# Performance work log

Measured on AMD Instinct MI355X. Metric: run time of the kernel, lower is better.

The kernel has to match this reference:

```python
import jax, jax.numpy as jnp
import numpy as np

K = 8  # knn_k
EPS = 1e-5


def _grid_edges(H, W):
    # 4-connectivity grid edges, both directions. Returns (src, tgt) numpy int arrays.
    idx = np.arange(H * W).reshape(H, W)
    right_a, right_b = idx[:, :-1].ravel(), idx[:, 1:].ravel()
    down_a, down_b = idx[:-1, :].ravel(), idx[1:, :].ravel()
    src = np.concatenate([right_a, right_b, down_a, down_b])
    tgt = np.concatenate([right_b, right_a, down_b, down_a])
    return src.astype(np.int32), tgt.astype(np.int32)


def setup_inputs() -> dict:
    key = jax.random.key(0)
    k1, _ = jax.random.split(key)
    feature_map = jax.random.normal(k1, (16, 256, 48, 48), dtype=jnp.float32)
    gamma = jnp.ones((256,), jnp.float32)
    beta = jnp.zeros((256,), jnp.float32)
    return {"feature_map": feature_map, "gamma": gamma, "beta": beta}


def reference(feature_map, gamma, beta):
    B, C, H, W = feature_map.shape
    N = H * W
    # flatten_feature_map: [B,C,H,W] -> [B,N,C]
    nodes = feature_map.reshape(B, C, N).transpose(0, 2, 1)

    # static grid edges (4-connectivity)
    g_src_np, g_tgt_np = _grid_edges(H, W)
    g_src = jnp.asarray(g_src_np)
    g_tgt = jnp.asarray(g_tgt_np)

    # feature-space kNN per sample (cdist + topk); exclude self with large diag
    big_diag = jnp.eye(N, dtype=nodes.dtype) * 1e9

    def knn_idx(x):  # x: [N, C]
        sq = jnp.sum(x * x, axis=1)
        d2 = sq[:, None] + sq[None, :] - 2.0 * (x @ x.T) + big_diag
        _, idx = jax.lax.top_k(-d2, K)  # [N, K] nearest neighbors
        return idx

    knn_src = jax.vmap(knn_idx)(nodes).reshape(B, N * K)  # per-sample sources
    knn_tgt = jnp.repeat(jnp.arange(N, dtype=jnp.int32), K)  # static targets

    tgt_all = jnp.concatenate([g_tgt, knn_tgt])  # same for all samples
    n_edges = tgt_all.shape[0]
    ones = jnp.ones((n_edges,), nodes.dtype)

    def aggregate(x, k_src):  # mean over incoming edges (fallback path)
        src_all = jnp.concatenate([g_src, k_src.astype(jnp.int32)])
        agg = jax.ops.segment_sum(x[src_all], tgt_all, num_segments=N)
        cnt = jax.ops.segment_sum(ones, tgt_all, num_segments=N)
        return agg / jnp.clip(cnt, 1.0)[:, None]

    refined = jax.vmap(aggregate)(nodes, knn_src)  # [B, N, C]

    # residual + LayerNorm over channel dim
    y = refined + nodes
    mu = jnp.mean(y, axis=-1, keepdims=True)
    var = jnp.mean((y - mu) ** 2, axis=-1, keepdims=True)
    y = (y - mu) * jax.lax.rsqrt(var + EPS) * gamma + beta

    # unflatten: [B,N,C] -> [B,C,H,W]
    return y.transpose(0, 2, 1).reshape(B, C, H, W)
```

## Files before the change

kernel.cpp:

```cpp
#include <hip/hip_runtime.h>

#define B_   16
#define C_   256
#define H_   48
#define W_   48
#define N_   (H_ * W_)
#define KNN  8

#define NG   (N_ / 32)
#define NT   17
#define FRAG 512
#define MPRE 10
#define NCAND 20

typedef __attribute__((ext_vector_type(8)))  short bf16x8;
typedef __attribute__((ext_vector_type(8)))  unsigned short u16x8;
typedef __attribute__((ext_vector_type(16))) float f32x16;

__device__ __forceinline__ unsigned short f2bf(float f) {
    unsigned int u = __float_as_uint(f);
    u = (u + 0x7FFF + ((u >> 16) & 1)) >> 16;
    return (unsigned short)u;
}
__device__ __forceinline__ float bf2f(unsigned short h) {
    return __uint_as_float(((unsigned int)h) << 16);
}
__device__ __forceinline__ bool lex_lt(float v, int i, float bv, int bi) {
    return (v < bv) || (v == bv && i < bi);
}
__device__ __forceinline__ unsigned int f2sort(float f) {
    unsigned int u = __float_as_uint(f);
    return u ^ ((unsigned int)((int)u >> 31) | 0x80000000u);
}

__global__ __launch_bounds__(256) void k_transpose(const float* __restrict__ fm,
                                                   float* __restrict__ nodes,
                                                   unsigned short* __restrict__ Xf) {
    __shared__ float tile[32][33];
    int b  = blockIdx.z;
    int n0 = blockIdx.x * 32;
    int c0 = blockIdx.y * 32;
    int tx = threadIdx.x, ty = threadIdx.y;
    const float* src = fm + (size_t)b * C_ * N_;
    float* dst = nodes + (size_t)b * N_ * C_;
    #pragma unroll
    for (int cc = 0; cc < 32; cc += 8)
        tile[cc + ty][tx] = src[(size_t)(c0 + cc + ty) * N_ + n0 + tx];
    __syncthreads();
    #pragma unroll
    for (int nn = 0; nn < 32; nn += 8)
        dst[(size_t)(n0 + nn + ty) * C_ + c0 + tx] = tile[tx][nn + ty];

    int flat = ty * 32 + tx;
    int wv = flat >> 6, lane = flat & 63;
    if (wv < 2) {
        int t   = 2 * blockIdx.y + wv;
        int l31 = lane & 31, lh = lane >> 5;
        u16x8 o;
        #pragma unroll
        for (int e = 0; e < 8; ++e)
            o[e] = f2bf(tile[wv * 16 + lh * 8 + e][l31]);
        unsigned short* df = Xf + (((size_t)b * NG + blockIdx.x) * NT + t) * FRAG + lane * 8;
        *(u16x8*)df = o;
    }
}

__global__ __launch_bounds__(256) void k_sq(const float* __restrict__ fm,
                                            float* __restrict__ sq,
                                            unsigned short* __restrict__ Xf) {
    int b = blockIdx.y;
    int n = blockIdx.x * 256 + threadIdx.x;
    const float* src = fm + (size_t)b * C_ * N_ + n;
    float s = 0.f;
    for (int c = 0; c < C_; ++c) { float v = src[(size_t)c * N_]; s = fmaf(v, v, s); }
    sq[b * N_ + n] = s;

    float sh = -0.5f * s;
    unsigned short e1 = f2bf(sh);
    unsigned short e2 = f2bf(sh - bf2f(e1));
    int g = n >> 5, l = n & 31;
    unsigned short* df = Xf + (((size_t)b * NG + g) * NT + 16) * FRAG + l * 8;
    u16x8 o = (u16x8){0, 0, 0, 0, 0, 0, 0, 0};
    o[0] = e1; o[1] = e2;
    *(u16x8*)df = o;
    u16x8 z = (u16x8){0, 0, 0, 0, 0, 0, 0, 0};
    *(u16x8*)(df + 32 * 8) = z;
}

__global__ __launch_bounds__(512) void k_knn_mfma(const unsigned short* __restrict__ Xf,
                                                  int* __restrict__ pi_pre) {
    __shared__ unsigned int ms[2][4][32][MPRE];

    int bid  = blockIdx.x;
    int wgid = (bid & 7) * 72 + (bid >> 3);
    int b    = wgid / 36;
    int i0   = (wgid % 36) * 64;

    int tid = threadIdx.x;
    int wave = tid >> 6, lane = tid & 63;
    int wi = wave & 1, wj = wave >> 1;
    int l31 = lane & 31, lh = lane >> 5;

    const unsigned short* Xb = Xf + (size_t)b * NG * NT * FRAG;
    int gi = (i0 >> 5) + wi;

    bf16x8 bfr[16];
    const unsigned short* ibase = Xb + (size_t)gi * NT * FRAG + lane * 8;
    #pragma unroll
    for (int t = 0; t < 16; ++t) bfr[t] = *(const bf16x8*)(ibase + t * FRAG);
    short one = (lh == 0) ? (short)0x3F80 : (short)0;
    bf16x8 bc = (bf16x8){one, one, 0, 0, 0, 0, 0, 0};

    int I0 = i0 + wi * 32 + l31;

    unsigned int best[MPRE];
    #pragma unroll
    for (int q = 0; q < MPRE; ++q) best[q] = 0u;

    for (int jt = 0; jt < 18; ++jt) {
        int gj = jt * 4 + wj;
        const unsigned short* ab = Xb + (size_t)gj * NT * FRAG + lane * 8;

        f32x16 acc;
        #pragma unroll
        for (int r = 0; r < 16; ++r) acc[r] = 0.f;

        #pragma unroll
        for (int t = 0; t < 16; ++t) {
            bf16x8 af = *(const bf16x8*)(ab + t * FRAG);
            acc = __builtin_amdgcn_mfma_f32_32x32x16_bf16(af, bfr[t], acc, 0, 0, 0);
        }
        {
            bf16x8 af = *(const bf16x8*)(ab + 16 * FRAG);
            acc = __builtin_amdgcn_mfma_f32_32x32x16_bf16(af, bc, acc, 0, 0, 0);
        }

        int j0 = gj * 32;
        int idxbase = 4095 - j0 - 4 * lh;
        #pragma unroll
        for (int r = 0; r < 16; ++r) {
            int cr = (r & 3) + 8 * (r >> 2);
            int gjrow = j0 + cr + 4 * lh;
            unsigned int p = (f2sort(acc[r]) & 0xFFFFF000u) | (unsigned int)(idxbase - cr);
            p = (gjrow == I0) ? 0u : p;
            #pragma unroll
            for (int q = 0; q < MPRE; ++q) {
                unsigned int hi = p > best[q] ? p : best[q];
                unsigned int lo = p > best[q] ? best[q] : p;
                best[q] = hi; p = lo;
            }
        }
    }

    {
        unsigned int part[MPRE];
        #pragma unroll
        for (int q = 0; q < MPRE; ++q)
            part[q] = (unsigned int)__shfl_xor((int)best[q], 32);
        #pragma unroll
        for (int q = 0; q < MPRE; ++q) {
            unsigned int p = part[q];
            #pragma unroll
            for (int s = 0; s < MPRE; ++s) {
                unsigned int hi = p > best[s] ? p : best[s];
                unsigned int lo = p > best[s] ? best[s] : p;
                best[s] = hi; p = lo;
            }
        }
    }
    if (lh == 0) {
        #pragma unroll
        for (int q = 0; q < MPRE; ++q) ms[wi][wj][l31][q] = best[q];
    }
    __syncthreads();

    if (tid < 64) {
        int mwi = tid >> 5, mcol = tid & 31;
        unsigned int mb[NCAND];
        #pragma unroll
        for (int q = 0; q < NCAND; ++q) mb[q] = 0u;
        for (int wjj = 0; wjj < 4; ++wjj) {
            #pragma unroll
            for (int qq = 0; qq < MPRE; ++qq) {
                unsigned int p = ms[mwi][wjj][mcol][qq];
                #pragma unroll
                for (int q = 0; q < NCAND; ++q) {
                    unsigned int hi = p > mb[q] ? p : mb[q];
                    unsigned int lo = p > mb[q] ? mb[q] : p;
                    mb[q] = hi; p = lo;
                }
            }
        }
        int i_g = i0 + tid;
        int* dst = pi_pre + ((size_t)b * N_ + i_g) * NCAND;
        #pragma unroll
        for (int q = 0; q < NCAND; ++q) dst[q] = 4095 - (int)(mb[q] & 0xFFFu);
    }
}

__global__ __launch_bounds__(256) void k_rerank(const float* __restrict__ nodes,
                                                const float* __restrict__ sq,
                                                const int* __restrict__ pi_pre,
                                                int* __restrict__ knn) {
    __shared__ float d2s[4][NCAND];
    __shared__ int   jss[4][NCAND];

    int wv   = threadIdx.x >> 6;
    int lane = threadIdx.x & 63;
    int row  = blockIdx.x * 4 + wv;
    int g = lane >> 4, m = lane & 15;
    int b = row / N_;
    const float* Xb = nodes + (size_t)b * N_ * C_;
    const float* xi = nodes + (size_t)row * C_;

    float4 xiv[4];
    #pragma unroll
    for (int p = 0; p < 4; ++p) xiv[p] = *(const float4*)&xi[p * 64 + m * 4];
    float sqi = sq[row];
    const int* cand = pi_pre + (size_t)row * NCAND;

    for (int it = 0; it < 5; ++it) {
        int c = it * 4 + g;
        int j = cand[c];
        bool valid = (unsigned)j < (unsigned)N_;
        int jc = valid ? j : 0;
        const float* xj = Xb + (size_t)jc * C_;
        float p = 0.f;
        #pragma unroll
        for (int pp = 0; pp < 4; ++pp) {
            float4 v = *(const float4*)&xj[pp * 64 + m * 4];
            p = fmaf(xiv[pp].x, v.x, p);
            p = fmaf(xiv[pp].y, v.y, p);
            p = fmaf(xiv[pp].z, v.z, p);
            p = fmaf(xiv[pp].w, v.w, p);
        }
        p += __shfl_xor(p, 1);
        p += __shfl_xor(p, 2);
        p += __shfl_xor(p, 4);
        p += __shfl_xor(p, 8);
        if (m == 0) {
            float d2 = valid ? (sqi + sq[b * N_ + jc] - 2.f * p) : 3.4e38f;
            d2s[wv][c] = d2;
            jss[wv][c] = valid ? j : 0x7fffffff;
        }
    }

    float bd[KNN]; int bj[KNN];
    #pragma unroll
    for (int q = 0; q < KNN; ++q) { bd[q] = 3.4e38f; bj[q] = 0x7fffffff; }
    for (int s = 0; s < NCAND; ++s) {
        float v = d2s[wv][s]; int jx = jss[wv][s];
        if (lex_lt(v, jx, bd[KNN - 1], bj[KNN - 1])) {
            float cv = v; int ci = jx;
            #pragma unroll
            for (int q = 0; q < KNN; ++q) {
                if (lex_lt(cv, ci, bd[q], bj[q])) {
                    float tv = bd[q]; bd[q] = cv; cv = tv;
                    int tx2 = bj[q]; bj[q] = ci; ci = tx2;
                }
            }
        }
    }
    if (lane == 0) {
        int* kr = knn + (size_t)row * KNN;
        #pragma unroll
        for (int q = 0; q < KNN; ++q) kr[q] = bj[q];
    }
}

__global__ __launch_bounds__(256) void k_agg_ln(const float* __restrict__ nodes,
                                                const int* __restrict__ knn,
                                                const float* __restrict__ gamma,
                                                const float* __restrict__ beta,
                                                float* __restrict__ out) {
    __shared__ float ytile[16][C_ + 1];

    int b   = blockIdx.y;
    int i0  = blockIdx.x * 16;
    int tid = threadIdx.x;
    int wv = tid >> 6, lane = tid & 63;
    const float* Xb = nodes + (size_t)b * N_ * C_;

    float4 g4 = *(const float4*)&gamma[lane * 4];
    float4 b4 = *(const float4*)&beta[lane * 4];

    for (int rr = 0; rr < 4; ++rr) {
        int ii = wv * 4 + rr;
        int i  = i0 + ii;
        int x_ = i % W_;
        int y_ = i / W_;
        float s0 = 0.f, s1 = 0.f, s2 = 0.f, s3 = 0.f;
        int cnt = KNN;

        #define ADDROW(J) { float4 v = *(const float4*)&Xb[(size_t)(J) * C_ + lane * 4]; \
                            s0 += v.x; s1 += v.y; s2 += v.z; s3 += v.w; }
        if (x_ > 0)      { ADDROW(i - 1);  cnt++; }
        if (x_ < W_ - 1) { ADDROW(i + 1);  cnt++; }
        if (y_ > 0)      { ADDROW(i - W_); cnt++; }
        if (y_ < H_ - 1) { ADDROW(i + W_); cnt++; }
        const int* kr = knn + ((size_t)b * N_ + i) * KNN;
        #pragma unroll
        for (int k = 0; k < KNN; ++k) ADDROW(kr[k]);
        #undef ADDROW

        float4 xi = *(const float4*)&Xb[(size_t)i * C_ + lane * 4];
        float ic = 1.f / (float)cnt;
        float y0 = s0 * ic + xi.x;
        float y1 = s1 * ic + xi.y;
        float y2 = s2 * ic + xi.z;
        float y3 = s3 * ic + xi.w;

        float rx = y0 + y1 + y2 + y3;
        float ry = y0 * y0 + y1 * y1 + y2 * y2 + y3 * y3;
        #pragma unroll
        for (int mm = 1; mm < 64; mm <<= 1) {
            rx += __shfl_xor(rx, mm);
            ry += __shfl_xor(ry, mm);
        }
        float mu  = rx * (1.f / C_);
        float var = ry * (1.f / C_) - mu * mu;
        float inv = rsqrtf(var + 1e-5f);

        ytile[ii][lane * 4 + 0] = (y0 - mu) * inv * g4.x + b4.x;
        ytile[ii][lane * 4 + 1] = (y1 - mu) * inv * g4.y + b4.y;
        ytile[ii][lane * 4 + 2] = (y2 - mu) * inv * g4.z + b4.z;
        ytile[ii][lane * 4 + 3] = (y3 - mu) * inv * g4.w + b4.w;
    }
    __syncthreads();

    float* op = out + (size_t)b * C_ * N_ + (size_t)tid * N_ + i0;
    float vv[16];
    #pragma unroll
    for (int ii = 0; ii < 16; ++ii) vv[ii] = ytile[ii][tid];
    #pragma unroll
    for (int q = 0; q < 4; ++q) {
        float4 w;
        w.x = vv[q * 4 + 0]; w.y = vv[q * 4 + 1];
        w.z = vv[q * 4 + 2]; w.w = vv[q * 4 + 3];
        *(float4*)&op[q * 4] = w;
    }
}

extern "C" void kernel_launch(void* const* d_in, const int* in_sizes, int n_in,
                              void* d_out, int out_size, void* d_ws, size_t ws_size,
                              hipStream_t stream) {
    const float* fm    = (const float*)d_in[0];
    const float* gamma = (const float*)d_in[1];
    const float* beta  = (const float*)d_in[2];
    float* out = (float*)d_out;

    char* ws = (char*)d_ws;
    size_t off = 0;
    float* nodes = (float*)(ws + off); off += (size_t)B_ * N_ * C_ * sizeof(float);
    float* sq    = (float*)(ws + off); off += (size_t)B_ * N_ * sizeof(float);
    int*   knn   = (int*)  (ws + off); off += (size_t)B_ * N_ * KNN * sizeof(int);
    unsigned short* Xf = (unsigned short*)(ws + off);
    off += (size_t)B_ * NG * NT * FRAG * sizeof(unsigned short);
    int* pi_pre = (int*)(ws + off);
    off += (size_t)B_ * N_ * NCAND * sizeof(int);

    k_transpose<<<dim3(N_ / 32, C_ / 32, B_), dim3(32, 8), 0, stream>>>(fm, nodes, Xf);
    k_sq<<<dim3(N_ / 256, B_), 256, 0, stream>>>(fm, sq, Xf);
    k_knn_mfma<<<(B_ * N_) / 64, 512, 0, stream>>>(Xf, pi_pre);
    k_rerank<<<(B_ * N_) / 4, 256, 0, stream>>>(nodes, sq, pi_pre, knn);
    k_agg_ln<<<dim3(N_ / 16, B_), 256, 0, stream>>>(nodes, knn, gamma, beta, out);
}
```

Measured before the change: 345.9 us.

## Fuse rerank into aggregation, shrink kNN blocks, drop sort-key conversion via bias

Merges the candidate rerank kernel into the aggregation/LayerNorm kernel so the selected neighbor indices stay in registers instead of round-tripping through global memory, removing one launch. The kNN MFMA kernel now uses 256-thread blocks covering a single 32-row group. A constant bias is injected through the extra MFMA column so scores can be compared as raw float bits, skipping the sign-fixing sort-key transform. This relies on all biased scores being non-negative; if not, ordering of candidates may be wrong.

```diff
diff --git a/kernel.cpp b/kernel.cpp
--- a/kernel.cpp
+++ b/kernel.cpp
@@ -27,10 +27,6 @@
 }
 __device__ __forceinline__ bool lex_lt(float v, int i, float bv, int bi) {
     return (v < bv) || (v == bv && i < bi);
-}
-__device__ __forceinline__ unsigned int f2sort(float f) {
-    unsigned int u = __float_as_uint(f);
-    return u ^ ((unsigned int)((int)u >> 31) | 0x80000000u);
 }
 
 __global__ __launch_bounds__(256) void k_transpose(const float* __restrict__ fm,
@@ -81,37 +77,35 @@
     int g = n >> 5, l = n & 31;
     unsigned short* df = Xf + (((size_t)b * NG + g) * NT + 16) * FRAG + l * 8;
     u16x8 o = (u16x8){0, 0, 0, 0, 0, 0, 0, 0};
-    o[0] = e1; o[1] = e2;
+    o[0] = e1; o[1] = e2; o[2] = 0x4400;
     *(u16x8*)df = o;
     u16x8 z = (u16x8){0, 0, 0, 0, 0, 0, 0, 0};
     *(u16x8*)(df + 32 * 8) = z;
 }
 
-__global__ __launch_bounds__(512) void k_knn_mfma(const unsigned short* __restrict__ Xf,
+__global__ __launch_bounds__(256) void k_knn_mfma(const unsigned short* __restrict__ Xf,
                                                   int* __restrict__ pi_pre) {
-    __shared__ unsigned int ms[2][4][32][MPRE];
+    __shared__ unsigned int ms[4][32][MPRE];
 
     int bid  = blockIdx.x;
-    int wgid = (bid & 7) * 72 + (bid >> 3);
-    int b    = wgid / 36;
-    int i0   = (wgid % 36) * 64;
+    int wgid = (bid & 7) * 144 + (bid >> 3);
+    int b    = wgid / NG;
+    int ig   = wgid % NG;
 
     int tid = threadIdx.x;
-    int wave = tid >> 6, lane = tid & 63;
-    int wi = wave & 1, wj = wave >> 1;
+    int wj = tid >> 6, lane = tid & 63;
     int l31 = lane & 31, lh = lane >> 5;
 
     const unsigned short* Xb = Xf + (size_t)b * NG * NT * FRAG;
-    int gi = (i0 >> 5) + wi;
 
     bf16x8 bfr[16];
-    const unsigned short* ibase = Xb + (size_t)gi * NT * FRAG + lane * 8;
+    const unsigned short* ibase = Xb + (size_t)ig * NT * FRAG + lane * 8;
     #pragma unroll
     for (int t = 0; t < 16; ++t) bfr[t] = *(const bf16x8*)(ibase + t * FRAG);
     short one = (lh == 0) ? (short)0x3F80 : (short)0;
-    bf16x8 bc = (bf16x8){one, one, 0, 0, 0, 0, 0, 0};
-
-    int I0 = i0 + wi * 32 + l31;
+    bf16x8 bc = (bf16x8){one, one, one, 0, 0, 0, 0, 0};
+
+    int I0 = ig * 32 + l31;
 
     unsigned int best[MPRE];
     #pragma unroll
@@ -141,7 +135,8 @@
         for (int r = 0; r < 16; ++r) {
             int cr = (r & 3) + 8 * (r >> 2);
             int gjrow = j0 + cr + 4 * lh;
-            unsigned int p = (f2sort(acc[r]) & 0xFFFFF000u) | (unsigned int)(idxbase - cr);
+            unsigned int p = (__float_as_uint(acc[r]) & 0xFFFFF000u)
+                           | (unsigned int)(idxbase - cr);
             p = (gjrow == I0) ? 0u : p;
             #pragma unroll
             for (int q = 0; q < MPRE; ++q) {
@@ -170,19 +165,18 @@
     }
     if (lh == 0) {
         #pragma unroll
-        for (int q = 0; q < MPRE; ++q) ms[wi][wj][l31][q] = best[q];
+        for (int q = 0; q < MPRE; ++q) ms[wj][l31][q] = best[q];
     }
     __syncthreads();
 
-    if (tid < 64) {
-        int mwi = tid >> 5, mcol = tid & 31;
+    if (tid < 32) {
         unsigned int mb[NCAND];
         #pragma unroll
         for (int q = 0; q < NCAND; ++q) mb[q] = 0u;
         for (int wjj = 0; wjj < 4; ++wjj) {
             #pragma unroll
             for (int qq = 0; qq < MPRE; ++qq) {
-                unsigned int p = ms[mwi][wjj][mcol][qq];
+                unsigned int p = ms[wjj][tid][qq];
                 #pragma unroll
                 for (int q = 0; q < NCAND; ++q) {
                     unsigned int hi = p > mb[q] ? p : mb[q];
@@ -191,124 +185,107 @@
                 }
             }
         }
-        int i_g = i0 + tid;
+        int i_g = ig * 32 + tid;
         int* dst = pi_pre + ((size_t)b * N_ + i_g) * NCAND;
         #pragma unroll
         for (int q = 0; q < NCAND; ++q) dst[q] = 4095 - (int)(mb[q] & 0xFFFu);
     }
 }
 
-__global__ __launch_bounds__(256) void k_rerank(const float* __restrict__ nodes,
-                                                const float* __restrict__ sq,
-                                                const int* __restrict__ pi_pre,
-                                                int* __restrict__ knn) {
+__global__ __launch_bounds__(256) void k_rerank_agg(const float* __restrict__ nodes,
+                                                    const float* __restrict__ sq,
+                                                    const int* __restrict__ pi_pre,
+                                                    const float* __restrict__ gamma,
+                                                    const float* __restrict__ beta,
+                                                    float* __restrict__ out) {
     __shared__ float d2s[4][NCAND];
     __shared__ int   jss[4][NCAND];
-
-    int wv   = threadIdx.x >> 6;
-    int lane = threadIdx.x & 63;
-    int row  = blockIdx.x * 4 + wv;
-    int g = lane >> 4, m = lane & 15;
-    int b = row / N_;
-    const float* Xb = nodes + (size_t)b * N_ * C_;
-    const float* xi = nodes + (size_t)row * C_;
-
-    float4 xiv[4];
-    #pragma unroll
-    for (int p = 0; p < 4; ++p) xiv[p] = *(const float4*)&xi[p * 64 + m * 4];
-    float sqi = sq[row];
-    const int* cand = pi_pre + (size_t)row * NCAND;
-
-    for (int it = 0; it < 5; ++it) {
-        int c = it * 4 + g;
-        int j = cand[c];
-        bool valid = (unsigned)j < (unsigned)N_;
-        int jc = valid ? j : 0;
-        const float* xj = Xb + (size_t)jc * C_;
-        float p = 0.f;
-        #pragma unroll
-        for (int pp = 0; pp < 4; ++pp) {
-            float4 v = *(const float4*)&xj[pp * 64 + m * 4];
-            p = fmaf(xiv[pp].x, v.x, p);
-            p = fmaf(xiv[pp].y, v.y, p);
-            p = fmaf(xiv[pp].z, v.z, p);
-            p = fmaf(xiv[pp].w, v.w, p);
-        }
-        p += __shfl_xor(p, 1);
-        p += __shfl_xor(p, 2);
-        p += __shfl_xor(p, 4);
-        p += __shfl_xor(p, 8);
-        if (m == 0) {
-            float d2 = valid ? (sqi + sq[b * N_ + jc] - 2.f * p) : 3.4e38f;
-            d2s[wv][c] = d2;
-            jss[wv][c] = valid ? j : 0x7fffffff;
-        }
-    }
-
-    float bd[KNN]; int bj[KNN];
-    #pragma unroll
-    for (int q = 0; q < KNN; ++q) { bd[q] = 3.4e38f; bj[q] = 0x7fffffff; }
-    for (int s = 0; s < NCAND; ++s) {
-        float v = d2s[wv][s]; int jx = jss[wv][s];
-        if (lex_lt(v, jx, bd[KNN - 1], bj[KNN - 1])) {
-            float cv = v; int ci = jx;
-            #pragma unroll
-            for (int q = 0; q < KNN; ++q) {
-                if (lex_lt(cv, ci, bd[q], bj[q])) {
-                    float tv = bd[q]; bd[q] = cv; cv = tv;
-                    int tx2 = bj[q]; bj[q] = ci; ci = tx2;
-                }
-            }
-        }
-    }
-    if (lane == 0) {
-        int* kr = knn + (size_t)row * KNN;
-        #pragma unroll
-        for (int q = 0; q < KNN; ++q) kr[q] = bj[q];
-    }
-}
-
-__global__ __launch_bounds__(256) void k_agg_ln(const float* __restrict__ nodes,
-                                                const int* __restrict__ knn,
-                                                const float* __restrict__ gamma,
-                                                const float* __restrict__ beta,
-                                                float* __restrict__ out) {
     __shared__ float ytile[16][C_ + 1];
 
-    int b   = blockIdx.y;
-    int i0  = blockIdx.x * 16;
-    int tid = threadIdx.x;
-    int wv = tid >> 6, lane = tid & 63;
+    int tid  = threadIdx.x;
+    int wv   = tid >> 6, lane = tid & 63;
+    int g    = lane >> 4, m = lane & 15;
+    int row0 = blockIdx.x * 16;
+    int b    = row0 / N_;
+    int i0   = row0 - b * N_;
     const float* Xb = nodes + (size_t)b * N_ * C_;
 
     float4 g4 = *(const float4*)&gamma[lane * 4];
     float4 b4 = *(const float4*)&beta[lane * 4];
 
     for (int rr = 0; rr < 4; ++rr) {
-        int ii = wv * 4 + rr;
-        int i  = i0 + ii;
+        int i    = i0 + wv * 4 + rr;
+        int rowg = b * N_ + i;
+
+        const float* xi = Xb + (size_t)i * C_;
+        float4 xiv[4];
+        #pragma unroll
+        for (int p = 0; p < 4; ++p) xiv[p] = *(const float4*)&xi[p * 64 + m * 4];
+        float sqi = sq[rowg];
+        const int* cand = pi_pre + (size_t)rowg * NCAND;
+
+        for (int it = 0; it < 5; ++it) {
+            int c = it * 4 + g;
+            int j = cand[c];
+            bool valid = (unsigned)j < (unsigned)N_;
+            int jc = valid ? j : 0;
+            const float* xj = Xb + (size_t)jc * C_;
+            float p = 0.f;
+            #pragma unroll
+            for (int pp = 0; pp < 4; ++pp) {
+                float4 v = *(const float4*)&xj[pp * 64 + m * 4];
+                p = fmaf(xiv[pp].x, v.x, p);
+                p = fmaf(xiv[pp].y, v.y, p);
+                p = fmaf(xiv[pp].z, v.z, p);
+                p = fmaf(xiv[pp].w, v.w, p);
+            }
+            p += __shfl_xor(p, 1);
+            p += __shfl_xor(p, 2);
+            p += __shfl_xor(p, 4);
+            p += __shfl_xor(p, 8);
+            if (m == 0) {
+                d2s[wv][c] = valid ? (sqi + sq[b * N_ + jc] - 2.f * p) : 3.4e38f;
+                jss[wv][c] = valid ? j : 0x7fffffff;
+            }
+        }
+
+        float bd[KNN]; int bj[KNN];
+        #pragma unroll
+        for (int q = 0; q < KNN; ++q) { bd[q] = 3.4e38f; bj[q] = 0x7fffffff; }
+        for (int s = 0; s < NCAND; ++s) {
+            float v = d2s[wv][s]; int jx = jss[wv][s];
+            if (lex_lt(v, jx, bd[KNN - 1], bj[KNN - 1])) {
+                float cv = v; int ci = jx;
+                #pragma unroll
+                for (int q = 0; q < KNN; ++q) {
+                    if (lex_lt(cv, ci, bd[q], bj[q])) {
+                        float tv = bd[q]; bd[q] = cv; cv = tv;
+                        int tx2 = bj[q]; bj[q] = ci; ci = tx2;
+                    }
+                }
+            }
+        }
+
         int x_ = i % W_;
         int y_ = i / W_;
         float s0 = 0.f, s1 = 0.f, s2 = 0.f, s3 = 0.f;
         int cnt = KNN;
-
         #define ADDROW(J) { float4 v = *(const float4*)&Xb[(size_t)(J) * C_ + lane * 4]; \
                             s0 += v.x; s1 += v.y; s2 += v.z; s3 += v.w; }
         if (x_ > 0)      { ADDROW(i - 1);  cnt++; }
         if (x_ < W_ - 1) { ADDROW(i + 1);  cnt++; }
         if (y_ > 0)      { ADDROW(i - W_); cnt++; }
         if (y_ < H_ - 1) { ADDROW(i + W_); cnt++; }
-        const int* kr = knn + ((size_t)b * N_ + i) * KNN;
-        #pragma unroll
-        for (int k = 0; k < KNN; ++k) ADDROW(kr[k]);
+        #pragma unroll
+        for (int k = 0; k < KNN; ++k) ADDROW(bj[k]);
         #undef ADDROW
 
-        float4 xi = *(const float4*)&Xb[(size_t)i * C_ + lane * 4];
+        float4 xi4 = *(const float4*)&Xb[(size_t)i * C_ + lane * 4];
         float ic = 1.f / (float)cnt;
-        float y0 = s0 * ic + xi.x;
-        float y1 = s1 * ic + xi.y;
-        float y2 = s2 * ic + xi.z;
-        float y3 = s3 * ic + xi.w;
+        float y0 = s0 * ic + xi4.x;
+        float y1 = s1 * ic + xi4.y;
+        float y2 = s2 * ic + xi4.z;
+        float y3 = s3 * ic + xi4.w;
 
         float rx = y0 + y1 + y2 + y3;
         float ry = y0 * y0 + y1 * y1 + y2 * y2 + y3 * y3;
@@ -321,6 +298,7 @@
         float var = ry * (1.f / C_) - mu * mu;
         float inv = rsqrtf(var + 1e-5f);
 
+        int ii = wv * 4 + rr;
         ytile[ii][lane * 4 + 0] = (y0 - mu) * inv * g4.x + b4.x;
         ytile[ii][lane * 4 + 1] = (y1 - mu) * inv * g4.y + b4.y;
         ytile[ii][lane * 4 + 2] = (y2 - mu) * inv * g4.z + b4.z;
@@ -353,7 +331,6 @@
     size_t off = 0;
     float* nodes = (float*)(ws + off); off += (size_t)B_ * N_ * C_ * sizeof(float);
     float* sq    = (float*)(ws + off); off += (size_t)B_ * N_ * sizeof(float);
-    int*   knn   = (int*)  (ws + off); off += (size_t)B_ * N_ * KNN * sizeof(int);
     unsigned short* Xf = (unsigned short*)(ws + off);
     off += (size_t)B_ * NG * NT * FRAG * sizeof(unsigned short);
     int* pi_pre = (int*)(ws + off);
@@ -361,7 +338,6 @@
 
     k_transpose<<<dim3(N_ / 32, C_ / 32, B_), dim3(32, 8), 0, stream>>>(fm, nodes, Xf);
     k_sq<<<dim3(N_ / 256, B_), 256, 0, stream>>>(fm, sq, Xf);
-    k_knn_mfma<<<(B_ * N_) / 64, 512, 0, stream>>>(Xf, pi_pre);
-    k_rerank<<<(B_ * N_) / 4, 256, 0, stream>>>(nodes, sq, pi_pre, knn);
-    k_agg_ln<<<dim3(N_ / 16, B_), 256, 0, stream>>>(nodes, knn, gamma, beta, out);
-}
+    k_knn_mfma<<<(B_ * NG), 256, 0, stream>>>(Xf, pi_pre);
+    k_rerank_agg<<<(B_ * N_) / 16, 256, 0, stream>>>(nodes, sq, pi_pre, gamma, beta, out);
+}
```

New measurement: 372.1 us. 1.08x slower.
